# Performance work log

Measured on AMD Instinct MI355X. Metric: run time of the kernel, lower is better.

## Reference

```python
import jax, jax.numpy as jnp
import numpy as np

N = 50000
E = 800000
D_IN = 256
HID = 64
HEADS = 4
OUT = 86
EPS_BN = 1e-5
NEG_SLOPE = 0.2


def setup_inputs() -> dict:
    key = jax.random.key(0)
    ks = jax.random.split(key, 16)
    HC = HEADS * HID
    inp = {
        "x": jax.random.normal(ks[0], (N, D_IN), jnp.float32),
        "edge_index": jax.random.randint(ks[1], (2, E), 0, N, jnp.int64),
        # GATConv 1: in=D_IN, out per head=HID, concat=True
        "W1": jax.random.normal(ks[2], (D_IN, HC), jnp.float32) * (1.0 / np.sqrt(D_IN)),
        "att_src1": jax.random.normal(ks[3], (HEADS, HID), jnp.float32) * 0.1,
        "att_dst1": jax.random.normal(ks[4], (HEADS, HID), jnp.float32) * 0.1,
        "b1": jnp.zeros((HC,), jnp.float32),
        # GATConv 2: in=HC, out per head=HID, concat=False (mean over heads)
        "W2": jax.random.normal(ks[5], (HC, HC), jnp.float32) * (1.0 / np.sqrt(HC)),
        "att_src2": jax.random.normal(ks[6], (HEADS, HID), jnp.float32) * 0.1,
        "att_dst2": jax.random.normal(ks[7], (HEADS, HID), jnp.float32) * 0.1,
        "b2": jnp.zeros((HID,), jnp.float32),
        # BatchNorms
        "g1": jnp.ones((HC,), jnp.float32),
        "be1": jnp.zeros((HC,), jnp.float32),
        "g2": jnp.ones((HID,), jnp.float32),
        "be2": jnp.zeros((HID,), jnp.float32),
        # PReLU (single shared weight, torch default init 0.25)
        "prelu_w": jnp.asarray(0.25, jnp.float32),
        # final Linear
        "fcW": jax.random.normal(ks[8], (HID, OUT), jnp.float32) * (1.0 / np.sqrt(HID)),
        "fcb": jnp.zeros((OUT,), jnp.float32),
    }
    return inp


def _gat_conv(x, src, dst, W, att_src, att_dst, bias, concat):
    # PyG GATConv forward (dropout inactive in eval mode).
    n = x.shape[0]
    H, C = att_src.shape
    h = (x @ W).reshape(n, H, C)                      # [N,H,C]
    a_s = jnp.sum(h * att_src[None], axis=-1)         # [N,H]
    a_d = jnp.sum(h * att_dst[None], axis=-1)         # [N,H]
    logits = jax.nn.leaky_relu(a_s[src] + a_d[dst], NEG_SLOPE)  # [E,H]
    # segment softmax over edges grouped by destination node
    m = jax.ops.segment_max(logits, dst, num_segments=n)        # [N,H]
    e = jnp.exp(logits - m[dst])
    s = jax.ops.segment_sum(e, dst, num_segments=n)             # [N,H]
    alpha = e / (s[dst] + 1e-16)                                # [E,H]
    msg = h[src] * alpha[:, :, None]                            # [E,H,C]
    out = jax.ops.segment_sum(msg, dst, num_segments=n)         # [N,H,C]
    if concat:
        return out.reshape(n, H * C) + bias
    return out.mean(axis=1) + bias


def _batch_norm(x, gamma, beta):
    mu = x.mean(axis=0)
    var = x.var(axis=0)
    return gamma * (x - mu) * jax.lax.rsqrt(var + EPS_BN) + beta


def reference(x, edge_index, W1, att_src1, att_dst1, b1, W2, att_src2, att_dst2, b2,
              g1, be1, g2, be2, prelu_w, fcW, fcb):
    n = x.shape[0]
    # GATConv default add_self_loops=True
    loops = jnp.arange(n, dtype=edge_index.dtype)
    src = jnp.concatenate([edge_index[0], loops])
    dst = jnp.concatenate([edge_index[1], loops])

    h = _gat_conv(x, src, dst, W1, att_src1, att_dst1, b1, concat=True)
    h = _batch_norm(h, g1, be1)
    h = jnp.where(h >= 0, h, prelu_w * h)             # PReLU
    # dropout: identity (eval)
    h = _gat_conv(h, src, dst, W2, att_src2, att_dst2, b2, concat=False)
    h = _batch_norm(h, g2, be2)
    h = jax.nn.elu(h)
    return h @ fcW + fcb
```

## Files before the change

kernel.cpp:

```cpp
#include <hip/hip_runtime.h>
#include <math.h>

#define LEAKY 0.2f

typedef __attribute__((ext_vector_type(8))) short short8;
typedef __attribute__((ext_vector_type(4))) float f32x4;

__device__ __forceinline__ float leaky02(float z) { return z >= 0.f ? z : LEAKY * z; }
__device__ __forceinline__ unsigned short f2bf(float f) {
  unsigned u = __float_as_uint(f);
  unsigned r = u + 0x7fffu + ((u >> 16) & 1u);
  return (unsigned short)(r >> 16);
}
__device__ __forceinline__ float bflo(unsigned u) { return __uint_as_float(u << 16); }
__device__ __forceinline__ float bfhi(unsigned u) { return __uint_as_float(u & 0xffff0000u); }

__global__ void count_kernel(const int* __restrict__ ei, int* __restrict__ cnt, int E, int N) {
  int e = blockIdx.x * 256 + threadIdx.x;
  int EP = E + N;
  if (e >= EP) return;
  int d = (e < E) ? ei[E + e] : (e - E);
  atomicAdd(&cnt[d], 1);
}

__global__ __launch_bounds__(256) void scan1_kernel(const int* __restrict__ cnt,
                                                    int* __restrict__ bsums, int n) {
  int i = blockIdx.x * 256 + threadIdx.x;
  int v = (i < n) ? cnt[i] : 0;
  int lane = threadIdx.x & 63, wv = threadIdx.x >> 6;
#pragma unroll
  for (int off = 32; off; off >>= 1) v += __shfl_xor(v, off);
  __shared__ int w[4];
  if (lane == 0) w[wv] = v;
  __syncthreads();
  if (threadIdx.x == 0) bsums[blockIdx.x] = w[0] + w[1] + w[2] + w[3];
}

__global__ __launch_bounds__(256) void scan2_kernel(int* __restrict__ bsums, int nb) {
  int tid = threadIdx.x;
  int lane = tid & 63, wv = tid >> 6;
  int v = (tid < nb) ? bsums[tid] : 0;
  int x = v;
#pragma unroll
  for (int off = 1; off < 64; off <<= 1) {
    int t = __shfl_up(x, off);
    if (lane >= off) x += t;
  }
  __shared__ int ws[4];
  if (lane == 63) ws[wv] = x;
  __syncthreads();
  int woff = 0;
#pragma unroll
  for (int w = 0; w < 4; ++w) if (w < wv) woff += ws[w];
  if (tid < nb) bsums[tid] = x + woff - v;
}

__global__ __launch_bounds__(256) void scan3_kernel(const int* __restrict__ cnt,
                                                    const int* __restrict__ boff,
                                                    int* __restrict__ rowptr,
                                                    int* __restrict__ cursor, int n) {
  int i = blockIdx.x * 256 + threadIdx.x;
  int tid = threadIdx.x, lane = tid & 63, wv = tid >> 6;
  int v = (i < n) ? cnt[i] : 0;
  int x = v;
#pragma unroll
  for (int off = 1; off < 64; off <<= 1) {
    int t = __shfl_up(x, off);
    if (lane >= off) x += t;
  }
  __shared__ int ws[4];
  if (lane == 63) ws[wv] = x;
  __syncthreads();
  int woff = 0;
#pragma unroll
  for (int w = 0; w < 4; ++w) if (w < wv) woff += ws[w];
  int incl = x + woff;
  int base = boff[blockIdx.x];
  if (i < n) {
    rowptr[i + 1] = base + incl;
    cursor[i] = base + incl - v;
  }
  if (i == 0) rowptr[0] = 0;
}

__global__ void fill_kernel(const int* __restrict__ ei, int* __restrict__ cursor,
                            int* __restrict__ srcs, int E, int N) {
  int e = blockIdx.x * 256 + threadIdx.x;
  int EP = E + N;
  if (e >= EP) return;
  int s, d;
  if (e < E) { s = ei[e]; d = ei[E + e]; } else { s = e - E; d = s; }
  int slot = atomicAdd(&cursor[d], 1);
  srcs[slot] = s;
}

__global__ void convw_kernel(const float* __restrict__ W1, const float* __restrict__ W2,
                             unsigned short* __restrict__ Wt1, unsigned short* __restrict__ Wt2) {
  int idx = blockIdx.x * 256 + threadIdx.x;
  const float* W;
  unsigned short* Wt;
  if (idx < 65536) { W = W1; Wt = Wt1; } else { W = W2; Wt = Wt2; idx -= 65536; }
  int c = idx >> 8, k = idx & 255;
  Wt[c * 256 + k] = f2bf(W[k * 256 + c]);
}

__global__ void convx_kernel(const float* __restrict__ x, unsigned short* __restrict__ xb,
                             int total) {
  int i = blockIdx.x * 256 + threadIdx.x;
  if (i * 8 >= total) return;
  float4 a = *(const float4*)&x[i * 8];
  float4 b = *(const float4*)&x[i * 8 + 4];
  ushort4 u0, u1;
  u0.x = f2bf(a.x); u0.y = f2bf(a.y); u0.z = f2bf(a.z); u0.w = f2bf(a.w);
  u1.x = f2bf(b.x); u1.y = f2bf(b.y); u1.z = f2bf(b.z); u1.w = f2bf(b.w);
  *(ushort4*)&xb[i * 8] = u0;
  *(ushort4*)&xb[i * 8 + 4] = u1;
}

__global__ __launch_bounds__(256) void gemm_kernel(const unsigned short* __restrict__ Ab,
                                                   const unsigned short* __restrict__ Wt,
                                                   unsigned short* __restrict__ Hout, int M,
                                                   const float* __restrict__ bnsc,
                                                   const float* __restrict__ bnsh,
                                                   const float* __restrict__ pwp,
                                                   const float* __restrict__ att_s,
                                                   const float* __restrict__ att_d,
                                                   float* __restrict__ as_o,
                                                   float* __restrict__ ad_o) {
  __shared__ unsigned short As[64][40];
  __shared__ unsigned short Bs[256][40];
  int tid = threadIdx.x;
  int bm = blockIdx.x * 64;
  int l = tid & 63, wv = tid >> 6;
  int lr = l & 15, lk = l >> 4;
  f32x4 acc[4][4] = {};
  bool hasbn = (bnsc != nullptr);
  float pws = pwp ? pwp[0] : 0.f;

  for (int k0 = 0; k0 < 256; k0 += 32) {
#pragma unroll
    for (int it = 0; it < 2; ++it) {
      int i = tid + it * 256;
      int row = i >> 3, kk = (i & 7) * 4;
      int gr = bm + row;
      uint2 u = make_uint2(0, 0);
      if (gr < M) u = *(const uint2*)&Ab[(size_t)gr * 256 + k0 + kk];
      if (hasbn) {
        float4 sc = *(const float4*)&bnsc[k0 + kk];
        float4 sh = *(const float4*)&bnsh[k0 + kk];
        float v0 = fmaf(bflo(u.x), sc.x, sh.x);
        float v1 = fmaf(bfhi(u.x), sc.y, sh.y);
        float v2 = fmaf(bflo(u.y), sc.z, sh.z);
        float v3 = fmaf(bfhi(u.y), sc.w, sh.w);
        v0 = v0 >= 0.f ? v0 : v0 * pws; v1 = v1 >= 0.f ? v1 : v1 * pws;
        v2 = v2 >= 0.f ? v2 : v2 * pws; v3 = v3 >= 0.f ? v3 : v3 * pws;
        ushort4 o;
        o.x = f2bf(v0); o.y = f2bf(v1); o.z = f2bf(v2); o.w = f2bf(v3);
        *(ushort4*)&As[row][kk] = o;
      } else {
        *(uint2*)&As[row][kk] = u;
      }
    }
#pragma unroll
    for (int it = 0; it < 8; ++it) {
      int i = tid + it * 256;
      int c = i >> 3, kk = (i & 7) * 4;
      *(uint2*)&Bs[c][kk] = *(const uint2*)&Wt[(size_t)c * 256 + k0 + kk];
    }
    __syncthreads();
    short8 af[4], bfr[4];
#pragma unroll
    for (int mt = 0; mt < 4; ++mt) af[mt] = *(const short8*)&As[mt * 16 + lr][lk * 8];
#pragma unroll
    for (int nt = 0; nt < 4; ++nt) bfr[nt] = *(const short8*)&Bs[wv * 64 + nt * 16 + lr][lk * 8];
#pragma unroll
    for (int mt = 0; mt < 4; ++mt)
#pragma unroll
      for (int nt = 0; nt < 4; ++nt)
        acc[mt][nt] = __builtin_amdgcn_mfma_f32_16x16x32_bf16(af[mt], bfr[nt], acc[mt][nt], 0, 0, 0);
    __syncthreads();
  }
  float asv[4], adv[4];
#pragma unroll
  for (int nt = 0; nt < 4; ++nt) {
    int gc = wv * 64 + nt * 16 + lr;
    asv[nt] = att_s[gc];
    adv[nt] = att_d[gc];
  }
#pragma unroll
  for (int mt = 0; mt < 4; ++mt) {
#pragma unroll
    for (int r = 0; r < 4; ++r) {
      int gr = bm + mt * 16 + lk * 4 + r;
      float ps = acc[mt][0][r] * asv[0] + acc[mt][1][r] * asv[1] +
                 acc[mt][2][r] * asv[2] + acc[mt][3][r] * asv[3];
      float pd = acc[mt][0][r] * adv[0] + acc[mt][1][r] * adv[1] +
                 acc[mt][2][r] * adv[2] + acc[mt][3][r] * adv[3];
#pragma unroll
      for (int off = 1; off < 16; off <<= 1) {
        ps += __shfl_xor(ps, off);
        pd += __shfl_xor(pd, off);
      }
      if (lr == 0 && gr < M) {
        as_o[gr * 4 + wv] = ps;
        ad_o[gr * 4 + wv] = pd;
      }
      if (gr < M) {
#pragma unroll
        for (int nt = 0; nt < 4; ++nt)
          Hout[(size_t)gr * 256 + wv * 64 + nt * 16 + lr] = f2bf(acc[mt][nt][r]);
      }
    }
  }
}

__global__ __launch_bounds__(256) void agg_kernel(const unsigned short* __restrict__ h,
                                                  const float* __restrict__ as_,
                                                  const float* __restrict__ ad_,
                                                  const int* __restrict__ rowptr,
                                                  const int* __restrict__ srcs,
                                                  const float* __restrict__ bias,
                                                  unsigned short* __restrict__ out_bf,
                                                  float* __restrict__ out_f,
                                                  int N, int concat) {
  int l = threadIdx.x & 63;
  int n = blockIdx.x * 4 + (threadIdx.x >> 6);
  if (n >= N) return;
  int e0 = rowptr[n], e1 = rowptr[n + 1];
  int deg = e1 - e0;
  int hh = l >> 4, le = l & 15;
  float adh = ad_[n * 4 + hh];

  if (deg <= 64) {
    int sidx[4];
    float lg[4];
#pragma unroll
    for (int t = 0; t < 4; ++t) {
      int j = e0 + le + 16 * t;
      if (j < e1) {
        int s = srcs[j];
        sidx[t] = s;
        lg[t] = leaky02(as_[s * 4 + hh] + adh);
      } else {
        sidx[t] = 0;
        lg[t] = -1e30f;
      }
    }
    float mx = fmaxf(fmaxf(lg[0], lg[1]), fmaxf(lg[2], lg[3]));
#pragma unroll
    for (int off = 1; off < 16; off <<= 1) mx = fmaxf(mx, __shfl_xor(mx, off));
    float ex[4];
    float sm = 0.f;
#pragma unroll
    for (int t = 0; t < 4; ++t) {
      ex[t] = (lg[t] > -1e29f) ? __expf(lg[t] - mx) : 0.f;
      sm += ex[t];
    }
#pragma unroll
    for (int off = 1; off < 16; off <<= 1) sm += __shfl_xor(sm, off);
    float inv = 1.f / (sm + 1e-16f);

    int p = l >> 5, m = l & 31;
    int hb = m >> 3;
    float invb = __shfl(inv, hb << 4);
    float a[8] = {0.f, 0.f, 0.f, 0.f, 0.f, 0.f, 0.f, 0.f};
#pragma unroll
    for (int t = 0; t < 4; ++t) {
      int base = e0 + 16 * t;
      if (base >= e1) break;
      int cntc = min(16, e1 - base);
      int npr = (cntc + 1) >> 1;
      for (int pr = 0; pr < npr; ++pr) {
        int q = 2 * pr + p;
        int s = __shfl(sidx[t], q);
        float al = __shfl(ex[t], q + (hb << 4)) * invb;
        uint4 hv = *(const uint4*)&h[(size_t)s * 256 + m * 8];
        a[0] = fmaf(bflo(hv.x), al, a[0]);
        a[1] = fmaf(bfhi(hv.x), al, a[1]);
        a[2] = fmaf(bflo(hv.y), al, a[2]);
        a[3] = fmaf(bfhi(hv.y), al, a[3]);
        a[4] = fmaf(bflo(hv.z), al, a[4]);
        a[5] = fmaf(bfhi(hv.z), al, a[5]);
        a[6] = fmaf(bflo(hv.w), al, a[6]);
        a[7] = fmaf(bfhi(hv.w), al, a[7]);
      }
    }
#pragma unroll
    for (int i = 0; i < 8; ++i) a[i] += __shfl_xor(a[i], 32);
    if (concat) {
      if (l < 32) {
        float4 b0 = *(const float4*)&bias[m * 8];
        float4 b1 = *(const float4*)&bias[m * 8 + 4];
        ushort4 o0, o1;
        o0.x = f2bf(a[0] + b0.x); o0.y = f2bf(a[1] + b0.y);
        o0.z = f2bf(a[2] + b0.z); o0.w = f2bf(a[3] + b0.w);
        o1.x = f2bf(a[4] + b1.x); o1.y = f2bf(a[5] + b1.y);
        o1.z = f2bf(a[6] + b1.z); o1.w = f2bf(a[7] + b1.w);
        *(ushort4*)&out_bf[(size_t)n * 256 + m * 8] = o0;
        *(ushort4*)&out_bf[(size_t)n * 256 + m * 8 + 4] = o1;
      }
    } else {
#pragma unroll
      for (int i = 0; i < 8; ++i) {
        a[i] += __shfl_xor(a[i], 8);
        a[i] += __shfl_xor(a[i], 16);
      }
      if (l < 8) {
        float4 b0 = *(const float4*)&bias[m * 8];
        float4 b1 = *(const float4*)&bias[m * 8 + 4];
        float4 o0 = make_float4(0.25f * a[0] + b0.x, 0.25f * a[1] + b0.y,
                                0.25f * a[2] + b0.z, 0.25f * a[3] + b0.w);
        float4 o1 = make_float4(0.25f * a[4] + b1.x, 0.25f * a[5] + b1.y,
                                0.25f * a[6] + b1.z, 0.25f * a[7] + b1.w);
        *(float4*)&out_f[(size_t)n * 64 + m * 8] = o0;
        *(float4*)&out_f[(size_t)n * 64 + m * 8 + 4] = o1;
      }
    }
  } else {
    float ad4[4] = {ad_[n * 4], ad_[n * 4 + 1], ad_[n * 4 + 2], ad_[n * 4 + 3]};
    float mx[4] = {-1e30f, -1e30f, -1e30f, -1e30f};
    for (int j = e0 + l; j < e1; j += 64) {
      int s = srcs[j];
      float4 av = *(const float4*)&as_[s * 4];
      mx[0] = fmaxf(mx[0], leaky02(av.x + ad4[0]));
      mx[1] = fmaxf(mx[1], leaky02(av.y + ad4[1]));
      mx[2] = fmaxf(mx[2], leaky02(av.z + ad4[2]));
      mx[3] = fmaxf(mx[3], leaky02(av.w + ad4[3]));
    }
#pragma unroll
    for (int off = 32; off; off >>= 1) {
      mx[0] = fmaxf(mx[0], __shfl_xor(mx[0], off));
      mx[1] = fmaxf(mx[1], __shfl_xor(mx[1], off));
      mx[2] = fmaxf(mx[2], __shfl_xor(mx[2], off));
      mx[3] = fmaxf(mx[3], __shfl_xor(mx[3], off));
    }
    float sm[4] = {0.f, 0.f, 0.f, 0.f};
    for (int j = e0 + l; j < e1; j += 64) {
      int s = srcs[j];
      float4 av = *(const float4*)&as_[s * 4];
      sm[0] += __expf(leaky02(av.x + ad4[0]) - mx[0]);
      sm[1] += __expf(leaky02(av.y + ad4[1]) - mx[1]);
      sm[2] += __expf(leaky02(av.z + ad4[2]) - mx[2]);
      sm[3] += __expf(leaky02(av.w + ad4[3]) - mx[3]);
    }
#pragma unroll
    for (int off = 32; off; off >>= 1) {
      sm[0] += __shfl_xor(sm[0], off);
      sm[1] += __shfl_xor(sm[1], off);
      sm[2] += __shfl_xor(sm[2], off);
      sm[3] += __shfl_xor(sm[3], off);
    }
    float mh = hh == 0 ? mx[0] : hh == 1 ? mx[1] : hh == 2 ? mx[2] : mx[3];
    float sh = hh == 0 ? sm[0] : hh == 1 ? sm[1] : hh == 2 ? sm[2] : sm[3];
    float inv = 1.f / (sh + 1e-16f);
    float a0 = 0.f, a1 = 0.f, a2 = 0.f, a3 = 0.f;
    for (int j = e0; j < e1; ++j) {
      int s = srcs[j];
      float al = __expf(leaky02(as_[s * 4 + hh] + adh) - mh) * inv;
      uint2 hv = *(const uint2*)&h[(size_t)s * 256 + l * 4];
      a0 = fmaf(bflo(hv.x), al, a0); a1 = fmaf(bfhi(hv.x), al, a1);
      a2 = fmaf(bflo(hv.y), al, a2); a3 = fmaf(bfhi(hv.y), al, a3);
    }
    if (concat) {
      float4 b4 = *(const float4*)&bias[l * 4];
      ushort4 o;
      o.x = f2bf(a0 + b4.x); o.y = f2bf(a1 + b4.y);
      o.z = f2bf(a2 + b4.z); o.w = f2bf(a3 + b4.w);
      *(ushort4*)&out_bf[(size_t)n * 256 + l * 4] = o;
    } else {
      a0 += __shfl_xor(a0, 16); a0 += __shfl_xor(a0, 32);
      a1 += __shfl_xor(a1, 16); a1 += __shfl_xor(a1, 32);
      a2 += __shfl_xor(a2, 16); a2 += __shfl_xor(a2, 32);
      a3 += __shfl_xor(a3, 16); a3 += __shfl_xor(a3, 32);
      if (l < 16) {
        float4 b4 = *(const float4*)&bias[l * 4];
        float4 o = make_float4(0.25f * a0 + b4.x, 0.25f * a1 + b4.y,
                               0.25f * a2 + b4.z, 0.25f * a3 + b4.w);
        *(float4*)&out_f[(size_t)n * 64 + l * 4] = o;
      }
    }
  }
}

__global__ __launch_bounds__(256) void bnstats_bf16_kernel(const unsigned short* __restrict__ x,
                                                           float* __restrict__ sum,
                                                           float* __restrict__ ss, int N) {
  int tid = threadIdx.x;
  int c = (tid & 127) * 2;
  int r = blockIdx.x * 2 + (tid >> 7);
  int stride = gridDim.x * 2;
  float a0 = 0.f, b0 = 0.f, a1 = 0.f, b1 = 0.f;
  for (; r < N; r += stride) {
    unsigned u = *(const unsigned*)&x[(size_t)r * 256 + c];
    float v0 = bflo(u), v1 = bfhi(u);
    a0 += v0; b0 += v0 * v0;
    a1 += v1; b1 += v1 * v1;
  }
  atomicAdd(&sum[c], a0); atomicAdd(&ss[c], b0);
  atomicAdd(&sum[c + 1], a1); atomicAdd(&ss[c + 1], b1);
}

__global__ __launch_bounds__(256) void bnstats_kernel(const float* __restrict__ x,
                                                      float* __restrict__ sum, float* __restrict__ ss,
                                                      int N, int C) {
  int tid = threadIdx.x;
  int f = tid % C;
  int rpb = 256 / C;
  int r = blockIdx.x * rpb + tid / C;
  int stride = gridDim.x * rpb;
  float a = 0.f, b = 0.f;
  for (; r < N; r += stride) {
    float v = x[(size_t)r * C + f];
    a += v;
    b += v * v;
  }
  atomicAdd(&sum[f], a);
  atomicAdd(&ss[f], b);
}

__global__ void bnfinalize_kernel(const float* __restrict__ sum, const float* __restrict__ ss,
                                  const float* __restrict__ gamma, const float* __restrict__ beta,
                                  float* __restrict__ scale, float* __restrict__ shift, int N, int C) {
  int f = threadIdx.x;
  if (f >= C) return;
  float mu = sum[f] / (float)N;
  float var = ss[f] / (float)N - mu * mu;
  float sc = gamma[f] * rsqrtf(var + 1e-5f);
  scale[f] = sc;
  shift[f] = beta[f] - mu * sc;
}

__global__ __launch_bounds__(256) void fc_kernel(const float* __restrict__ x,
                                                 const float* __restrict__ sc, const float* __restrict__ sh,
                                                 const float* __restrict__ W, const float* __restrict__ b,
                                                 float* __restrict__ out, int N) {
  __shared__ float ws[64 * 86];
  __shared__ float xs[32 * 64];
  int tid = threadIdx.x;
  for (int i = tid; i < 64 * 86; i += 256) ws[i] = W[i];
  int n0 = blockIdx.x * 32;
  for (int i = tid; i < 32 * 64; i += 256) {
    int n = n0 + (i >> 6), c = i & 63;
    float v = (n < N) ? x[(size_t)n * 64 + c] : 0.f;
    v = fmaf(v, sc[c], sh[c]);
    xs[i] = v > 0.f ? v : expm1f(v);
  }
  __syncthreads();
  for (int idx = tid; idx < 32 * 86; idx += 256) {
    int nl = idx / 86, o = idx % 86;
    int n = n0 + nl;
    if (n >= N) continue;
    float acc = b[o];
    const float* xr = &xs[nl * 64];
#pragma unroll 8
    for (int k = 0; k < 64; ++k) acc = fmaf(xr[k], ws[k * 86 + o], acc);
    out[(size_t)n * 86 + o] = acc;
  }
}

extern "C" void kernel_launch(void* const* d_in, const int* in_sizes, int n_in,
                              void* d_out, int out_size, void* d_ws, size_t ws_size,
                              hipStream_t stream) {
  const float* x    = (const float*)d_in[0];
  const int*   ei   = (const int*)d_in[1];
  const float* W1   = (const float*)d_in[2];
  const float* asw1 = (const float*)d_in[3];
  const float* adw1 = (const float*)d_in[4];
  const float* b1   = (const float*)d_in[5];
  const float* W2   = (const float*)d_in[6];
  const float* asw2 = (const float*)d_in[7];
  const float* adw2 = (const float*)d_in[8];
  const float* b2   = (const float*)d_in[9];
  const float* g1   = (const float*)d_in[10];
  const float* be1  = (const float*)d_in[11];
  const float* g2   = (const float*)d_in[12];
  const float* be2  = (const float*)d_in[13];
  const float* pw   = (const float*)d_in[14];
  const float* fcW  = (const float*)d_in[15];
  const float* fcb  = (const float*)d_in[16];

  const int N = in_sizes[0] / 256;
  const int E = in_sizes[1] / 2;
  const int EP = E + N;

  char* ws = (char*)d_ws;
  size_t off = 0;
  auto alloc = [&](size_t bytes) {
    char* p = ws + off;
    off += (bytes + 255) & ~(size_t)255;
    return p;
  };
  unsigned short* xb   = (unsigned short*)alloc((size_t)N * 256 * 2);
  unsigned short* h    = (unsigned short*)alloc((size_t)N * 256 * 2);
  unsigned short* outb = (unsigned short*)alloc((size_t)N * 256 * 2);
  float* xm   = (float*)alloc((size_t)N * 64 * 4);
  float* as1  = (float*)alloc((size_t)N * 4 * 4);
  float* ad1  = (float*)alloc((size_t)N * 4 * 4);
  float* as2  = (float*)alloc((size_t)N * 4 * 4);
  float* ad2  = (float*)alloc((size_t)N * 4 * 4);
  int* rowptr = (int*)alloc((size_t)(N + 1) * 4);
  int* cnt    = (int*)alloc((size_t)N * 4);
  int* cursor = (int*)alloc((size_t)N * 4);
  int* srcs   = (int*)alloc((size_t)EP * 4);
  int* bsums  = (int*)alloc(1024 * 4);
  unsigned short* Wt1 = (unsigned short*)alloc(65536 * 2);
  unsigned short* Wt2 = (unsigned short*)alloc(65536 * 2);
  float* bstat = (float*)alloc(512 * 4);
  float* bsum = bstat, *bss = bstat + 256;
  float* bsc  = (float*)alloc(256 * 4);
  float* bsh  = (float*)alloc(256 * 4);
  float* bsc2 = (float*)alloc(64 * 4);
  float* bsh2 = (float*)alloc(64 * 4);

  int egrid = (EP + 255) / 256;
  int ngrid4 = (N + 3) / 4;
  int nb = (N + 255) / 256;
  int ggrid = (N + 63) / 64;

  hipMemsetAsync(cnt, 0, (size_t)N * 4, stream);
  count_kernel<<<egrid, 256, 0, stream>>>(ei, cnt, E, N);
  convw_kernel<<<512, 256, 0, stream>>>(W1, W2, Wt1, Wt2);
  convx_kernel<<<(N * 32 + 255) / 256, 256, 0, stream>>>(x, xb, N * 256);
  scan1_kernel<<<nb, 256, 0, stream>>>(cnt, bsums, N);
  scan2_kernel<<<1, 256, 0, stream>>>(bsums, nb);
  scan3_kernel<<<nb, 256, 0, stream>>>(cnt, bsums, rowptr, cursor, N);
  fill_kernel<<<egrid, 256, 0, stream>>>(ei, cursor, srcs, E, N);

  gemm_kernel<<<ggrid, 256, 0, stream>>>(xb, Wt1, h, N, nullptr, nullptr, nullptr,
                                         asw1, adw1, as1, ad1);
  agg_kernel<<<ngrid4, 256, 0, stream>>>(h, as1, ad1, rowptr, srcs, b1, outb, nullptr, N, 1);

  hipMemsetAsync(bstat, 0, 512 * 4, stream);
  bnstats_bf16_kernel<<<512, 256, 0, stream>>>(outb, bsum, bss, N);
  bnfinalize_kernel<<<1, 256, 0, stream>>>(bsum, bss, g1, be1, bsc, bsh, N, 256);

  gemm_kernel<<<ggrid, 256, 0, stream>>>(outb, Wt2, h, N, bsc, bsh, pw,
                                         asw2, adw2, as2, ad2);
  agg_kernel<<<ngrid4, 256, 0, stream>>>(h, as2, ad2, rowptr, srcs, b2, nullptr, xm, N, 0);

  hipMemsetAsync(bstat, 0, 128 * 4, stream);
  bnstats_kernel<<<512, 256, 0, stream>>>(xm, bstat, bstat + 64, N, 64);
  bnfinalize_kernel<<<1, 64, 0, stream>>>(bstat, bstat + 64, g2, be2, bsc2, bsh2, N, 64);

  fc_kernel<<<(N + 31) / 32, 256, 0, stream>>>(xm, bsc2, bsh2, fcW, fcb, (float*)d_out, N);
}
```

Baseline: 586.4 us.

## Fuse fp32-to-bf16 input conversion into GEMM and double GEMM row tile

Removes the separate convx kernel and its bf16 copy of x. The first GEMM now reads fp32 x directly and converts it while staging into shared memory. The GEMM also moves to 128-row tiles with 512 threads (8 waves laid out 2x4), so each W tile load is reused across twice as many rows and loads are 16 bytes wide. The trade-off is that the first GEMM reads twice the A bytes, and the larger blocks may lower occupancy.

```diff
diff --git a/kernel.cpp b/kernel.cpp
--- a/kernel.cpp
+++ b/kernel.cpp
@@ -104,20 +104,8 @@
   Wt[c * 256 + k] = f2bf(W[k * 256 + c]);
 }
 
-__global__ void convx_kernel(const float* __restrict__ x, unsigned short* __restrict__ xb,
-                             int total) {
-  int i = blockIdx.x * 256 + threadIdx.x;
-  if (i * 8 >= total) return;
-  float4 a = *(const float4*)&x[i * 8];
-  float4 b = *(const float4*)&x[i * 8 + 4];
-  ushort4 u0, u1;
-  u0.x = f2bf(a.x); u0.y = f2bf(a.y); u0.z = f2bf(a.z); u0.w = f2bf(a.w);
-  u1.x = f2bf(b.x); u1.y = f2bf(b.y); u1.z = f2bf(b.z); u1.w = f2bf(b.w);
-  *(ushort4*)&xb[i * 8] = u0;
-  *(ushort4*)&xb[i * 8 + 4] = u1;
-}
-
-__global__ __launch_bounds__(256) void gemm_kernel(const unsigned short* __restrict__ Ab,
+template <bool BF16A>
+__global__ __launch_bounds__(512) void gemm_kernel(const void* __restrict__ Av,
                                                    const unsigned short* __restrict__ Wt,
                                                    unsigned short* __restrict__ Hout, int M,
                                                    const float* __restrict__ bnsc,
@@ -127,52 +115,74 @@
                                                    const float* __restrict__ att_d,
                                                    float* __restrict__ as_o,
                                                    float* __restrict__ ad_o) {
-  __shared__ unsigned short As[64][40];
+  __shared__ unsigned short As[128][40];
   __shared__ unsigned short Bs[256][40];
   int tid = threadIdx.x;
-  int bm = blockIdx.x * 64;
+  int bm = blockIdx.x * 128;
   int l = tid & 63, wv = tid >> 6;
+  int wm = wv >> 2, wn = wv & 3;
   int lr = l & 15, lk = l >> 4;
   f32x4 acc[4][4] = {};
   bool hasbn = (bnsc != nullptr);
   float pws = pwp ? pwp[0] : 0.f;
 
   for (int k0 = 0; k0 < 256; k0 += 32) {
+    {
+      int row = tid >> 2, kq = (tid & 3) * 8;
+      int gr = bm + row;
+      if (BF16A) {
+        uint4 u = make_uint4(0, 0, 0, 0);
+        if (gr < M) u = *(const uint4*)((const unsigned short*)Av + (size_t)gr * 256 + k0 + kq);
+        if (hasbn) {
+          float4 sc0 = *(const float4*)&bnsc[k0 + kq];
+          float4 sh0 = *(const float4*)&bnsh[k0 + kq];
+          float4 sc1 = *(const float4*)&bnsc[k0 + kq + 4];
+          float4 sh1 = *(const float4*)&bnsh[k0 + kq + 4];
+          float v0 = fmaf(bflo(u.x), sc0.x, sh0.x);
+          float v1 = fmaf(bfhi(u.x), sc0.y, sh0.y);
+          float v2 = fmaf(bflo(u.y), sc0.z, sh0.z);
+          float v3 = fmaf(bfhi(u.y), sc0.w, sh0.w);
+          float v4 = fmaf(bflo(u.z), sc1.x, sh1.x);
+          float v5 = fmaf(bfhi(u.z), sc1.y, sh1.y);
+          float v6 = fmaf(bflo(u.w), sc1.z, sh1.z);
+          float v7 = fmaf(bfhi(u.w), sc1.w, sh1.w);
+          v0 = v0 >= 0.f ? v0 : v0 * pws; v1 = v1 >= 0.f ? v1 : v1 * pws;
+          v2 = v2 >= 0.f ? v2 : v2 * pws; v3 = v3 >= 0.f ? v3 : v3 * pws;
+          v4 = v4 >= 0.f ? v4 : v4 * pws; v5 = v5 >= 0.f ? v5 : v5 * pws;
+          v6 = v6 >= 0.f ? v6 : v6 * pws; v7 = v7 >= 0.f ? v7 : v7 * pws;
+          ushort4 o0, o1;
+          o0.x = f2bf(v0); o0.y = f2bf(v1); o0.z = f2bf(v2); o0.w = f2bf(v3);
+          o1.x = f2bf(v4); o1.y = f2bf(v5); o1.z = f2bf(v6); o1.w = f2bf(v7);
+          *(ushort4*)&As[row][kq] = o0;
+          *(ushort4*)&As[row][kq + 4] = o1;
+        } else {
+          *(uint4*)&As[row][kq] = u;
+        }
+      } else {
+        float4 a0 = make_float4(0.f, 0.f, 0.f, 0.f), a1 = a0;
+        if (gr < M) {
+          a0 = *(const float4*)((const float*)Av + (size_t)gr * 256 + k0 + kq);
+          a1 = *(const float4*)((const float*)Av + (size_t)gr * 256 + k0 + kq + 4);
+        }
+        ushort4 o0, o1;
+        o0.x = f2bf(a0.x); o0.y = f2bf(a0.y); o0.z = f2bf(a0.z); o0.w = f2bf(a0.w);
+        o1.x = f2bf(a1.x); o1.y = f2bf(a1.y); o1.z = f2bf(a1.z); o1.w = f2bf(a1.w);
+        *(ushort4*)&As[row][kq] = o0;
+        *(ushort4*)&As[row][kq + 4] = o1;
+      }
+    }
 #pragma unroll
     for (int it = 0; it < 2; ++it) {
-      int i = tid + it * 256;
-      int row = i >> 3, kk = (i & 7) * 4;
-      int gr = bm + row;
-      uint2 u = make_uint2(0, 0);
-      if (gr < M) u = *(const uint2*)&Ab[(size_t)gr * 256 + k0 + kk];
-      if (hasbn) {
-        float4 sc = *(const float4*)&bnsc[k0 + kk];
-        float4 sh = *(const float4*)&bnsh[k0 + kk];
-        float v0 = fmaf(bflo(u.x), sc.x, sh.x);
-        float v1 = fmaf(bfhi(u.x), sc.y, sh.y);
-        float v2 = fmaf(bflo(u.y), sc.z, sh.z);
-        float v3 = fmaf(bfhi(u.y), sc.w, sh.w);
-        v0 = v0 >= 0.f ? v0 : v0 * pws; v1 = v1 >= 0.f ? v1 : v1 * pws;
-        v2 = v2 >= 0.f ? v2 : v2 * pws; v3 = v3 >= 0.f ? v3 : v3 * pws;
-        ushort4 o;
-        o.x = f2bf(v0); o.y = f2bf(v1); o.z = f2bf(v2); o.w = f2bf(v3);
-        *(ushort4*)&As[row][kk] = o;
-      } else {
-        *(uint2*)&As[row][kk] = u;
-      }
-    }
-#pragma unroll
-    for (int it = 0; it < 8; ++it) {
-      int i = tid + it * 256;
-      int c = i >> 3, kk = (i & 7) * 4;
-      *(uint2*)&Bs[c][kk] = *(const uint2*)&Wt[(size_t)c * 256 + k0 + kk];
+      int i = tid + it * 512;
+      int c = i >> 2, kq = (i & 3) * 8;
+      *(uint4*)&Bs[c][kq] = *(const uint4*)&Wt[(size_t)c * 256 + k0 + kq];
     }
     __syncthreads();
     short8 af[4], bfr[4];
 #pragma unroll
-    for (int mt = 0; mt < 4; ++mt) af[mt] = *(const short8*)&As[mt * 16 + lr][lk * 8];
-#pragma unroll
-    for (int nt = 0; nt < 4; ++nt) bfr[nt] = *(const short8*)&Bs[wv * 64 + nt * 16 + lr][lk * 8];
+    for (int mt = 0; mt < 4; ++mt) af[mt] = *(const short8*)&As[wm * 64 + mt * 16 + lr][lk * 8];
+#pragma unroll
+    for (int nt = 0; nt < 4; ++nt) bfr[nt] = *(const short8*)&Bs[wn * 64 + nt * 16 + lr][lk * 8];
 #pragma unroll
     for (int mt = 0; mt < 4; ++mt)
 #pragma unroll
@@ -183,7 +193,7 @@
   float asv[4], adv[4];
 #pragma unroll
   for (int nt = 0; nt < 4; ++nt) {
-    int gc = wv * 64 + nt * 16 + lr;
+    int gc = wn * 64 + nt * 16 + lr;
     asv[nt] = att_s[gc];
     adv[nt] = att_d[gc];
   }
@@ -191,7 +201,7 @@
   for (int mt = 0; mt < 4; ++mt) {
 #pragma unroll
     for (int r = 0; r < 4; ++r) {
-      int gr = bm + mt * 16 + lk * 4 + r;
+      int gr = bm + wm * 64 + mt * 16 + lk * 4 + r;
       float ps = acc[mt][0][r] * asv[0] + acc[mt][1][r] * asv[1] +
                  acc[mt][2][r] * asv[2] + acc[mt][3][r] * asv[3];
       float pd = acc[mt][0][r] * adv[0] + acc[mt][1][r] * adv[1] +
@@ -202,13 +212,13 @@
         pd += __shfl_xor(pd, off);
       }
       if (lr == 0 && gr < M) {
-        as_o[gr * 4 + wv] = ps;
-        ad_o[gr * 4 + wv] = pd;
+        as_o[gr * 4 + wn] = ps;
+        ad_o[gr * 4 + wn] = pd;
       }
       if (gr < M) {
 #pragma unroll
         for (int nt = 0; nt < 4; ++nt)
-          Hout[(size_t)gr * 256 + wv * 64 + nt * 16 + lr] = f2bf(acc[mt][nt][r]);
+          Hout[(size_t)gr * 256 + wn * 64 + nt * 16 + lr] = f2bf(acc[mt][nt][r]);
       }
     }
   }
@@ -490,7 +500,6 @@
     off += (bytes + 255) & ~(size_t)255;
     return p;
   };
-  unsigned short* xb   = (unsigned short*)alloc((size_t)N * 256 * 2);
   unsigned short* h    = (unsigned short*)alloc((size_t)N * 256 * 2);
   unsigned short* outb = (unsigned short*)alloc((size_t)N * 256 * 2);
   float* xm   = (float*)alloc((size_t)N * 64 * 4);
@@ -515,27 +524,26 @@
   int egrid = (EP + 255) / 256;
   int ngrid4 = (N + 3) / 4;
   int nb = (N + 255) / 256;
-  int ggrid = (N + 63) / 64;
+  int ggrid = (N + 127) / 128;
 
   hipMemsetAsync(cnt, 0, (size_t)N * 4, stream);
   count_kernel<<<egrid, 256, 0, stream>>>(ei, cnt, E, N);
   convw_kernel<<<512, 256, 0, stream>>>(W1, W2, Wt1, Wt2);
-  convx_kernel<<<(N * 32 + 255) / 256, 256, 0, stream>>>(x, xb, N * 256);
   scan1_kernel<<<nb, 256, 0, stream>>>(cnt, bsums, N);
   scan2_kernel<<<1, 256, 0, stream>>>(bsums, nb);
   scan3_kernel<<<nb, 256, 0, stream>>>(cnt, bsums, rowptr, cursor, N);
   fill_kernel<<<egrid, 256, 0, stream>>>(ei, cursor, srcs, E, N);
 
-  gemm_kernel<<<ggrid, 256, 0, stream>>>(xb, Wt1, h, N, nullptr, nullptr, nullptr,
-                                         asw1, adw1, as1, ad1);
+  gemm_kernel<false><<<ggrid, 512, 0, stream>>>(x, Wt1, h, N, nullptr, nullptr, nullptr,
+                                                asw1, adw1, as1, ad1);
   agg_kernel<<<ngrid4, 256, 0, stream>>>(h, as1, ad1, rowptr, srcs, b1, outb, nullptr, N, 1);
 
   hipMemsetAsync(bstat, 0, 512 * 4, stream);
   bnstats_bf16_kernel<<<512, 256, 0, stream>>>(outb, bsum, bss, N);
   bnfinalize_kernel<<<1, 256, 0, stream>>>(bsum, bss, g1, be1, bsc, bsh, N, 256);
 
-  gemm_kernel<<<ggrid, 256, 0, stream>>>(outb, Wt2, h, N, bsc, bsh, pw,
-                                         asw2, adw2, as2, ad2);
+  gemm_kernel<true><<<ggrid, 512, 0, stream>>>(outb, Wt2, h, N, bsc, bsh, pw,
+                                               asw2, adw2, as2, ad2);
   agg_kernel<<<ngrid4, 256, 0, stream>>>(h, as2, ad2, rowptr, srcs, b2, nullptr, xm, N, 0);
 
   hipMemsetAsync(bstat, 0, 128 * 4, stream);
```

Result: faster. 565.8 us (-3.5%).
